# Kernel tuning notes

Measured on AMD Instinct MI355X. Metric: run time of the kernel, lower is better.

## Reference

```python
import jax, jax.numpy as jnp
import numpy as np

K = 1024
D = 64
BETA = 0.25
DECAY = 0.99
EPS = 1e-05


def setup_inputs() -> dict:
    key = jax.random.key(0)
    k1, k2 = jax.random.split(key)
    z = jax.random.normal(k1, (32, D, 64, 64), dtype=jnp.float32)
    # nn.init.uniform_(weight, -1/K, 1/K)
    embedding = jax.random.uniform(k2, (K, D), dtype=jnp.float32, minval=-1.0 / K, maxval=1.0 / K)
    # post-_maybe_init_ema_from_embedding state
    cluster_size = jnp.ones((K,), dtype=jnp.float32)
    embed_avg = embedding.copy()
    return {"z": z, "embedding": embedding, "cluster_size": cluster_size, "embed_avg": embed_avg}


def reference(z, embedding, cluster_size, embed_avg):
    B, C, H, W = z.shape
    z_nhwc = jnp.transpose(z, (0, 2, 3, 1))            # [B,H,W,D]
    flat = z_nhwc.reshape(-1, D)                        # [N,D]

    x2 = jnp.sum(flat * flat, axis=1, keepdims=True)    # [N,1]
    w2 = jnp.sum(embedding * embedding, axis=1)         # [K]
    dist = x2 + w2[None, :] - 2.0 * flat @ embedding.T  # [N,K]
    idx = jnp.argmin(dist, axis=1)                      # [N] int

    z_q = embedding[idx].reshape(z_nhwc.shape)          # gather

    # EMA codebook update (training, update=True)
    counts = jax.ops.segment_sum(jnp.ones_like(idx, dtype=jnp.float32), idx, num_segments=K)
    embed_sum = jax.ops.segment_sum(flat, idx, num_segments=K)  # [K,D]
    new_cluster_size = cluster_size * DECAY + (1.0 - DECAY) * counts
    new_embed_avg = embed_avg * DECAY + (1.0 - DECAY) * embed_sum
    n = jnp.sum(new_cluster_size)
    smoothed = (new_cluster_size + EPS) / (n + K * EPS) * n
    new_embedding = new_embed_avg / smoothed[:, None]

    # commitment loss (z_q detached) + straight-through estimator
    loss = BETA * jnp.mean((z_nhwc - jax.lax.stop_gradient(z_q)) ** 2)
    z_q_ste = z_nhwc + jax.lax.stop_gradient(z_q - z_nhwc)
    z_q_out = jnp.transpose(z_q_ste, (0, 3, 1, 2))      # back to [B,C,H,W]
    return (z_q_out, idx, loss, new_embedding, new_cluster_size, new_embed_avg)
```

## Files before the change

kernel.cpp:

```cpp
#include <hip/hip_runtime.h>
#include <hip/hip_bf16.h>

#define NROWS 131072
#define DDIM  64
#define KCODES 1024
#define HW    4096

#define OFF_ZQ   0ull
#define OFF_IDX  8388608ull
#define OFF_LOSS 8519680ull
#define OFF_EMB  8519681ull
#define OFF_NCS  8585217ull
#define OFF_EAVG 8586241ull

#define SCR_B0    34078724ull
#define SCR_WLO   (SCR_B0 + 131072ull)
#define SCR_W2O   (SCR_B0 + 262144ull)
#define LCAP      20480u

#define FWS_KSCR   16777216ull
#define FWS_ES     16777216ull
#define FWS_CNTF   17039360ull
#define FWS_SX2    17043456ull
#define FWS_SMOOTH 17047552ull
#define FWS_LIST   17301504ull
#define FWS_RMIN   17383424ull
#define FWS_CNTR   17547264ull
#define FWS_TOTAL  17547268ull

#define WSO_KSCR   262144ull
#define WSO_LOSSB  786432ull
#define WSO_SMOOTH 788480ull
#define WSO_CNT    792576ull
#define WSO_ESUM   858112ull

#define GAPTHR 8e-5f

typedef __attribute__((ext_vector_type(8))) short bf16x8;
typedef __attribute__((ext_vector_type(4))) float f32x4;

__device__ __forceinline__ float np_sumsq64(const float* v) {
#pragma clang fp contract(off)
    float r0 = v[0]*v[0], r1 = v[1]*v[1], r2 = v[2]*v[2], r3 = v[3]*v[3];
    float r4 = v[4]*v[4], r5 = v[5]*v[5], r6 = v[6]*v[6], r7 = v[7]*v[7];
    for (int i = 8; i < 64; i += 8) {
        r0 += v[i+0]*v[i+0]; r1 += v[i+1]*v[i+1];
        r2 += v[i+2]*v[i+2]; r3 += v[i+3]*v[i+3];
        r4 += v[i+4]*v[i+4]; r5 += v[i+5]*v[i+5];
        r6 += v[i+6]*v[i+6]; r7 += v[i+7]*v[i+7];
    }
    return ((r0+r1)+(r2+r3))+((r4+r5)+(r6+r7));
}
__device__ __forceinline__ float mul_rn(float a, float b) {
#pragma clang fp contract(off)
    return a * b;
}
__device__ __forceinline__ float add_rn(float a, float b) {
#pragma clang fp contract(off)
    return a + b;
}
__device__ __forceinline__ float sub2_rn(float s, float a) {
#pragma clang fp contract(off)
    return s - 2.0f * a;
}
__device__ __forceinline__ unsigned bf16rne(float v) {
    unsigned b = __float_as_uint(v);
    return (b + 0x7FFFu + ((b >> 16) & 1u)) >> 16;
}
__device__ __forceinline__ float bfu2f(unsigned short u) {
    return __uint_as_float(((unsigned)u) << 16);
}
__device__ __forceinline__ unsigned flipf(float v) {
    unsigned b = __float_as_uint(v);
    return b ^ (0x80000000u | (unsigned)((int)b >> 31));
}
__device__ __forceinline__ float unflip_val(unsigned u) {
    u &= 0xFFFFFC00u;
    unsigned mask = 0x80000000u | (unsigned)((int)(~u) >> 31);
    return __uint_as_float(u ^ mask);
}

__global__ __launch_bounds__(256) void prep_kernel(
        const float* __restrict__ emb, unsigned short* __restrict__ wh,
        unsigned short* __restrict__ wl, float* __restrict__ w2,
        float* __restrict__ embT) {
    __shared__ float tile[64][65];
    const int t = threadIdx.x;
    const int kb = blockIdx.x * 64;
#pragma unroll
    for (int i = 0; i < 16; ++i) {
        const int e = t + i * 256;
        const int kl = e >> 6, d = e & 63;
        const float v = emb[(size_t)(kb + kl) * DDIM + d];
        tile[kl][d] = v;
        const unsigned rh = bf16rne(v);
        const float lv = v - bfu2f((unsigned short)rh);
        wh[(size_t)(kb + kl) * DDIM + d] = (unsigned short)rh;
        wl[(size_t)(kb + kl) * DDIM + d] = (unsigned short)bf16rne(lv);
    }
    __syncthreads();
    if (t < 64) w2[kb + t] = np_sumsq64(&tile[t][0]);
#pragma unroll
    for (int i = 0; i < 16; ++i) {
        const int e = t + i * 256;
        const int d = e >> 6, kl = e & 63;
        embT[(size_t)d * KCODES + kb + kl] = tile[kl][d];
    }
}

#define CBLOAD(S, c)                                                          \
    { const size_t a_ = ((size_t)(((c) * 16 + col) * DDIM + grp * 8));        \
      wh##S##0 = *(const bf16x8*)(wh + a_);                                   \
      wh##S##1 = *(const bf16x8*)(wh + a_ + 32);                              \
      wl##S##0 = *(const bf16x8*)(wl + a_);                                   \
      wl##S##1 = *(const bf16x8*)(wl + a_ + 32); }

#define CBCOMP4(S, c)                                                         \
    { const float4 w2v = *(const float4*)&w2g[(c) * 16 + grp * 4];            \
      const float* w2p = (const float*)&w2v;                                  \
      _Pragma("unroll")                                                       \
      for (int rt = 0; rt < 4; ++rt) {                                        \
        f32x4 aA = {0.f,0.f,0.f,0.f}, aB = {0.f,0.f,0.f,0.f};                 \
        aA = __builtin_amdgcn_mfma_f32_16x16x32_bf16(wh##S##0, fx[rt][0], aA, 0, 0, 0); \
        aA = __builtin_amdgcn_mfma_f32_16x16x32_bf16(wl##S##0, fx[rt][0], aA, 0, 0, 0); \
        aB = __builtin_amdgcn_mfma_f32_16x16x32_bf16(wh##S##1, fx[rt][1], aB, 0, 0, 0); \
        aB = __builtin_amdgcn_mfma_f32_16x16x32_bf16(wl##S##1, fx[rt][1], aB, 0, 0, 0); \
        _Pragma("unroll")                                                     \
        for (int r = 0; r < 4; ++r) {                                         \
          const float val = fmaf(-2.f, aA[r] + aB[r], w2p[r]);                \
          const unsigned u = (flipf(val) & 0xFFFFFC00u) |                     \
                             (unsigned)((c) * 16 + grp * 4 + r);              \
          const unsigned mx = m1[rt] > u ? m1[rt] : u;                        \
          m1[rt] = m1[rt] < u ? m1[rt] : u;                                   \
          m2[rt] = m2[rt] < mx ? m2[rt] : mx;                                 \
        } } }

__global__ __launch_bounds__(512, 4) void score2_kernel(
        const float* __restrict__ z,
        const unsigned short* __restrict__ wh, const unsigned short* __restrict__ wl,
        const float* __restrict__ w2g, float* __restrict__ out,
        unsigned short* __restrict__ xT, unsigned* __restrict__ list,
        unsigned long long* __restrict__ rmin, unsigned* __restrict__ counter) {
    __shared__ __attribute__((aligned(16))) unsigned short sxt[64][512];

    const int tid = threadIdx.x;
    const int lane = tid & 63, wid = tid >> 6;
    const int col = lane & 15, grp = lane >> 4;
    const int nb = blockIdx.x * 512;
    const int b = nb >> 12, hb = (nb >> 6) & 63;

    {
        const int w4 = (tid & 15) * 4, h = (tid >> 4) & 7, dg = tid >> 7;
#pragma unroll
        for (int j = 0; j < 16; ++j) {
            const int d = dg * 16 + j;
            const float4 v = *(const float4*)&z[((size_t)(b * 64 + d)) * HW + (hb + h) * 64 + w4];
            ushort4 u;
            u.x = (unsigned short)bf16rne(v.x);
            u.y = (unsigned short)bf16rne(v.y);
            u.z = (unsigned short)bf16rne(v.z);
            u.w = (unsigned short)bf16rne(v.w);
            *(ushort4*)&sxt[d][h * 64 + w4] = u;
        }
    }
    __syncthreads();

    bf16x8 fx[4][2];
#pragma unroll
    for (int rt = 0; rt < 4; ++rt)
#pragma unroll
        for (int kh = 0; kh < 2; ++kh) {
            const int row = wid * 64 + rt * 16 + col;
            bf16x8 f;
#pragma unroll
            for (int j = 0; j < 8; ++j)
                f[j] = (short)sxt[kh * 32 + grp * 8 + j][row];
            fx[rt][kh] = f;
            *(bf16x8*)&xT[(size_t)(nb + row) * DDIM + kh * 32 + grp * 8] = f;
        }

    unsigned m1[4] = {~0u, ~0u, ~0u, ~0u}, m2[4] = {~0u, ~0u, ~0u, ~0u};
    bf16x8 whA0, whA1, wlA0, wlA1, whB0, whB1, wlB0, wlB1;

    CBLOAD(A, 0)
    for (int c = 0; c < 64; c += 2) {
        CBLOAD(B, c + 1)
        CBCOMP4(A, c)
        if (c + 2 < 64) CBLOAD(A, c + 2)
        CBCOMP4(B, c + 1)
    }

#pragma unroll
    for (int rt = 0; rt < 4; ++rt) {
        for (int off = 16; off <= 32; off <<= 1) {
            const unsigned o1 = (unsigned)__shfl_xor((int)m1[rt], off, 64);
            const unsigned o2 = (unsigned)__shfl_xor((int)m2[rt], off, 64);
            const unsigned mx = m1[rt] > o1 ? m1[rt] : o1;
            m1[rt] = m1[rt] < o1 ? m1[rt] : o1;
            const unsigned t2 = m2[rt] < o2 ? m2[rt] : o2;
            m2[rt] = t2 < mx ? t2 : mx;
        }
    }

    bool flag[4];
    unsigned long long mrt[4];
    unsigned wavecnt = 0;
#pragma unroll
    for (int rt = 0; rt < 4; ++rt) {
        flag[rt] = (grp == 0) &&
                   ((unflip_val(m2[rt]) - unflip_val(m1[rt])) < GAPTHR);
        mrt[rt] = __ballot(flag[rt]);
        wavecnt += (unsigned)__popcll(mrt[rt]);
    }

    if (grp == 0) {
#pragma unroll
        for (int rt = 0; rt < 4; ++rt)
            out[OFF_IDX + (size_t)(nb + wid * 64 + rt * 16 + col)] =
                (float)(m1[rt] & 1023u);
    }

    unsigned base = 0;
    if (lane == 0 && wavecnt) base = atomicAdd(counter, wavecnt);
    base = (unsigned)__shfl((int)base, 0, 64);
    unsigned offrt = 0;
#pragma unroll
    for (int rt = 0; rt < 4; ++rt) {
        if (flag[rt]) {
            const unsigned offin =
                (unsigned)__popcll(mrt[rt] & ((lane == 0) ? 0ull : (~0ull >> (64 - lane))));
            const unsigned slot = base + offrt + offin;
            if (slot < LCAP) {
                list[slot] = (unsigned)(nb + wid * 64 + rt * 16 + col);
                rmin[slot] = ~0ull;
            }
        }
        offrt += (unsigned)__popcll(mrt[rt]);
    }
}

__global__ __launch_bounds__(256, 1) void rescanb_kernel(
        const float* __restrict__ z, const float* __restrict__ emb,
        const float* __restrict__ w2, const unsigned* __restrict__ list,
        const unsigned* __restrict__ counter,
        unsigned long long* __restrict__ rmin) {
    const int lane = threadIdx.x & 63;
    const int wid = __builtin_amdgcn_readfirstlane(threadIdx.x >> 6);
    unsigned cnt = __builtin_amdgcn_readfirstlane(*counter);
    if (cnt > LCAP) cnt = LCAP;
    if (cnt == 0) return;
    const unsigned W = ((cnt + 63) >> 6) * 8;

    for (unsigned w = blockIdx.x * 4 + wid; w < W; w += gridDim.x * 4) {
        const unsigned g = w >> 3, p = w & 7;
        const unsigned slot = g * 64 + lane;
        const bool valid = slot < cnt;
        const unsigned n = list[valid ? slot : 0];
        const unsigned hw = n & 4095u, bb = n >> 12;

        float x[64];
#pragma unroll
        for (int d = 0; d < 64; ++d)
            x[d] = z[(size_t)(bb * 64 + d) * (size_t)HW + hw];

        float r[8];
#pragma unroll
        for (int j = 0; j < 8; ++j) r[j] = mul_rn(x[j], x[j]);
#pragma unroll
        for (int i = 8; i < 64; i += 8)
#pragma unroll
            for (int j = 0; j < 8; ++j)
                r[j] = add_rn(r[j], mul_rn(x[i + j], x[i + j]));
        const float x2 = add_rn(add_rn(add_rn(r[0], r[1]), add_rn(r[2], r[3])),
                                add_rn(add_rn(r[4], r[5]), add_rn(r[6], r[7])));

        unsigned long long best = ~0ull;
        const int k0 = (int)p * 128;
        for (int k = k0; k < k0 + 128; k += 2) {
            const float* wa = emb + (size_t)k * DDIM;
            const float* wb = wa + DDIM;
            float aa = 0.f, ab = 0.f;
#pragma unroll
            for (int d = 0; d < 64; ++d) {
                aa = fmaf(x[d], wa[d], aa);
                ab = fmaf(x[d], wb[d], ab);
            }
            const float da = sub2_rn(add_rn(x2, w2[k]),     aa);
            const float db = sub2_rn(add_rn(x2, w2[k + 1]), ab);
            const unsigned long long ua =
                ((unsigned long long)flipf(da) << 10) | (unsigned long long)k;
            const unsigned long long ub =
                ((unsigned long long)flipf(db) << 10) | (unsigned long long)(k + 1);
            best = best < ua ? best : ua;
            best = best < ub ? best : ub;
        }
        if (valid) atomicMin(&rmin[slot], best);
    }
}

__global__ __launch_bounds__(256) void fix_kernel(
        const unsigned* __restrict__ list, const unsigned long long* __restrict__ rmin,
        const unsigned* __restrict__ counter, float* __restrict__ out) {
    unsigned cnt = *counter;
    if (cnt > LCAP) cnt = LCAP;
    const unsigned t = blockIdx.x * 256 + threadIdx.x;
    if (t < cnt) {
        const unsigned long long u = rmin[t];
        if (u != ~0ull)
            out[OFF_IDX + (size_t)list[t]] = (float)(unsigned)(u & 1023ull);
    }
}

__global__ __launch_bounds__(256) void gather_kernel(
        const float* __restrict__ idxf, const unsigned short* __restrict__ xT,
        float* __restrict__ es, float* __restrict__ cntf, float* __restrict__ sx2a) {
    const int k = blockIdx.x;
    const int lane = threadIdx.x & 63, wid = threadIdx.x >> 6;
    const float fk = (float)k;
    float acc = 0.f, s2 = 0.f;
    unsigned cnt = 0;
    const int wbase = wid * 32768;

    float4 cur = *(const float4*)&idxf[wbase + lane * 4];
    for (int it = 0; it < 128; ++it) {
        float4 nxt;
        if (it + 1 < 128)
            nxt = *(const float4*)&idxf[wbase + (it + 1) * 256 + lane * 4];
        const float* cp = (const float*)&cur;
#pragma unroll
        for (int j = 0; j < 4; ++j) {
            unsigned long long m = __ballot(cp[j] == fk);
            cnt += (unsigned)__popcll(m);
            while (m) {
                const int src = __ffsll(m) - 1;
                m &= m - 1;
                const int n = wbase + it * 256 + src * 4 + j;
                const float xv = bfu2f(xT[(size_t)n * DDIM + lane]);
                acc += xv;
                s2 = fmaf(xv, xv, s2);
            }
        }
        cur = nxt;
    }
#pragma unroll
    for (int off = 32; off > 0; off >>= 1) s2 += __shfl_down(s2, off, 64);
    __shared__ float sacc[4][64];
    __shared__ float ssx2[4];
    __shared__ unsigned scnt[4];
    sacc[wid][lane] = acc;
    if (lane == 0) { ssx2[wid] = s2; scnt[wid] = cnt; }
    __syncthreads();
    if (wid == 0) {
        const float t = sacc[0][lane] + sacc[1][lane] + sacc[2][lane] + sacc[3][lane];
        es[(size_t)k * DDIM + lane] = t;
        if (lane == 0) {
            cntf[k] = (float)(scnt[0] + scnt[1] + scnt[2] + scnt[3]);
            sx2a[k] = ssx2[0] + ssx2[1] + ssx2[2] + ssx2[3];
        }
    }
}

__global__ __launch_bounds__(512, 4) void zq_kernel(
        const float* __restrict__ emb, const float* __restrict__ idxf,
        float* __restrict__ out) {
    __shared__ unsigned k1s[256];
    const int tid = threadIdx.x;
    const int lane = tid & 63, wid = tid >> 6;
    const int nb = blockIdx.x * 256;
    const int b = nb >> 12, hb = (nb >> 6) & 63;
    if (tid < 256) k1s[tid] = (unsigned)idxf[nb + tid];
    __syncthreads();

    const int h = lane >> 4, w4 = (lane & 15) * 4;
    const int row = h * 64 + w4;
    const float* e0 = emb + (size_t)k1s[row + 0] * DDIM;
    const float* e1 = emb + (size_t)k1s[row + 1] * DDIM;
    const float* e2 = emb + (size_t)k1s[row + 2] * DDIM;
    const float* e3 = emb + (size_t)k1s[row + 3] * DDIM;
#pragma unroll
    for (int it = 0; it < 8; ++it) {
        const int d = wid + 8 * it;
        float4 q;
        q.x = e0[d]; q.y = e1[d]; q.z = e2[d]; q.w = e3[d];
        *(float4*)&out[((size_t)(b * 64 + d)) * HW + (hb + h) * 64 + w4] = q;
    }
}

__global__ __launch_bounds__(1024) void fin1_f(
        const float* __restrict__ cs, const float* __restrict__ emb,
        float* __restrict__ out, const float* __restrict__ w2,
        const float* __restrict__ es, const float* __restrict__ cntf,
        const float* __restrict__ sx2a, float* __restrict__ smoothed) {
    const int k = threadIdx.x;
    const float cnt = cntf[k];
    const float w2k = w2[k];
    const float* ek = es + (size_t)k * DDIM;
    const float* wk = emb + (size_t)k * DDIM;
    float dt = 0.f;
#pragma unroll
    for (int d = 0; d < DDIM; ++d) dt = fmaf(ek[d], wk[d], dt);
    const float lp = sx2a[k] - 2.f * dt + cnt * w2k;
    const float ncs = fmaf(0.01f, cnt, 0.99f * cs[k]);

    __shared__ float red[1024];
    red[k] = ncs;
    __syncthreads();
    for (int s = 512; s > 0; s >>= 1) {
        if (k < s) red[k] += red[k + s];
        __syncthreads();
    }
    const float nn = red[0];
    __syncthreads();
    red[k] = lp;
    __syncthreads();
    for (int s = 512; s > 0; s >>= 1) {
        if (k < s) red[k] += red[k + s];
        __syncthreads();
    }
    smoothed[k] = (ncs + 1e-5f) / (nn + 1024.f * 1e-5f) * nn;
    out[OFF_NCS + (size_t)k] = ncs;
    if (k == 0) out[OFF_LOSS] = 0.25f * red[0] / 8388608.f;
}

__global__ __launch_bounds__(256) void fin2_f(
        const float* __restrict__ eavg, float* __restrict__ out,
        const float* __restrict__ es, const float* __restrict__ smoothed) {
    const int e = blockIdx.x * 256 + threadIdx.x;
    const float ea = fmaf(0.01f, es[e], 0.99f * eavg[e]);
    out[OFF_EAVG + (size_t)e] = ea;
    out[OFF_EMB  + (size_t)e] = ea / smoothed[e >> 6];
}


#define CBCOMP(S, c)                                                          \
    { const float4 w2v = *(const float4*)&w2s[(c) * 16 + grp * 4];            \
      const float* w2p = (const float*)&w2v;                                  \
      _Pragma("unroll")                                                       \
      for (int rt = 0; rt < 2; ++rt) {                                        \
        f32x4 aA = {0.f,0.f,0.f,0.f}, aB = {0.f,0.f,0.f,0.f};                 \
        aA = __builtin_amdgcn_mfma_f32_16x16x32_bf16(wh##S##0, fx[rt][0], aA, 0, 0, 0); \
        aA = __builtin_amdgcn_mfma_f32_16x16x32_bf16(wl##S##0, fx[rt][0], aA, 0, 0, 0); \
        aB = __builtin_amdgcn_mfma_f32_16x16x32_bf16(wh##S##1, fx[rt][1], aB, 0, 0, 0); \
        aB = __builtin_amdgcn_mfma_f32_16x16x32_bf16(wl##S##1, fx[rt][1], aB, 0, 0, 0); \
        _Pragma("unroll")                                                     \
        for (int r = 0; r < 4; ++r) {                                         \
          const float val = fmaf(-2.f, aA[r] + aB[r], w2p[r]);                \
          const unsigned u = (flipf(val) & 0xFFFFFC00u) |                     \
                             (unsigned)((c) * 16 + grp * 4 + r);              \
          const unsigned mx = m1[rt] > u ? m1[rt] : u;                        \
          m1[rt] = m1[rt] < u ? m1[rt] : u;                                   \
          m2[rt] = m2[rt] < mx ? m2[rt] : mx;                                 \
        } } }

__global__ __launch_bounds__(512, 4) void score_kernel(
        const float* __restrict__ z,
        const unsigned short* __restrict__ wh, const unsigned short* __restrict__ wl,
        const float* __restrict__ w2, unsigned* __restrict__ kscr) {
    __shared__ __attribute__((aligned(16))) unsigned short sxt[64][260];
    __shared__ float w2s[KCODES];

    const int tid = threadIdx.x;
    const int lane = tid & 63, wid = tid >> 6;
    const int col = lane & 15, grp = lane >> 4;
    const int nb = blockIdx.x * 256;
    const int b = nb >> 12, hb = (nb >> 6) & 63;

    for (int i = tid; i < KCODES; i += 512) w2s[i] = w2[i];
    {
        const int h = lane >> 4, w4 = (lane & 15) * 4;
        const int row = h * 64 + w4;
#pragma unroll
        for (int it = 0; it < 8; ++it) {
            const int d = wid + 8 * it;
            const float4 v = *(const float4*)&z[((size_t)(b * 64 + d)) * HW + (hb + h) * 64 + w4];
            ushort4 u;
            u.x = (unsigned short)bf16rne(v.x);
            u.y = (unsigned short)bf16rne(v.y);
            u.z = (unsigned short)bf16rne(v.z);
            u.w = (unsigned short)bf16rne(v.w);
            *(ushort4*)&sxt[d][row] = u;
        }
    }
    __syncthreads();

    bf16x8 fx[2][2];
#pragma unroll
    for (int rt = 0; rt < 2; ++rt)
#pragma unroll
        for (int kh = 0; kh < 2; ++kh) {
            const int row = wid * 32 + rt * 16 + col;
            bf16x8 f;
#pragma unroll
            for (int j = 0; j < 8; ++j)
                f[j] = (short)sxt[kh * 32 + grp * 8 + j][row];
            fx[rt][kh] = f;
        }

    unsigned m1[2] = {~0u, ~0u}, m2[2] = {~0u, ~0u};
    bf16x8 whA0, whA1, wlA0, wlA1, whB0, whB1, wlB0, wlB1;

    CBLOAD(A, 0)
    for (int c = 0; c < 64; c += 2) {
        CBLOAD(B, c + 1)
        CBCOMP(A, c)
        if (c + 2 < 64) CBLOAD(A, c + 2)
        CBCOMP(B, c + 1)
    }
#pragma unroll
    for (int rt = 0; rt < 2; ++rt) {
        for (int off = 16; off <= 32; off <<= 1) {
            const unsigned o1 = (unsigned)__shfl_xor((int)m1[rt], off, 64);
            const unsigned o2 = (unsigned)__shfl_xor((int)m2[rt], off, 64);
            const unsigned mx = m1[rt] > o1 ? m1[rt] : o1;
            m1[rt] = m1[rt] < o1 ? m1[rt] : o1;
            const unsigned t2 = m2[rt] < o2 ? m2[rt] : o2;
            m2[rt] = t2 < mx ? t2 : mx;
        }
        if (grp == 0) {
            const bool fl = (unflip_val(m2[rt]) - unflip_val(m1[rt])) < GAPTHR;
            kscr[nb + wid * 32 + rt * 16 + col] =
                (m1[rt] & 1023u) | (fl ? 0x80000000u : 0u);
        }
    }
}

__global__ __launch_bounds__(512, 4) void output_kernel(
        const float* __restrict__ z, const float* __restrict__ emb,
        const float* __restrict__ embT, const float* __restrict__ w2,
        float* __restrict__ out, const unsigned* __restrict__ kscr,
        float* __restrict__ esum_p, unsigned* __restrict__ cnt_p,
        float* __restrict__ lossb, int pmask) {
    __shared__ __attribute__((aligned(16))) unsigned short sxt[64][260];
    __shared__ unsigned k1s[256];
    __shared__ float redl[8];

    const int tid = threadIdx.x;
    const int lane = tid & 63, wid = tid >> 6;
    const int nb = blockIdx.x * 256;
    const int b = nb >> 12, hb = (nb >> 6) & 63;

    {
        const int h = lane >> 4, w4 = (lane & 15) * 4;
        const int row = h * 64 + w4;
#pragma unroll
        for (int it = 0; it < 8; ++it) {
            const int d = wid + 8 * it;
            const float4 v = *(const float4*)&z[((size_t)(b * 64 + d)) * HW + (hb + h) * 64 + w4];
            ushort4 u;
            u.x = (unsigned short)bf16rne(v.x);
            u.y = (unsigned short)bf16rne(v.y);
            u.z = (unsigned short)bf16rne(v.z);
            u.w = (unsigned short)bf16rne(v.w);
            *(ushort4*)&sxt[d][row] = u;
        }
    }

    unsigned kf = 0;
    if (lane < 32) kf = kscr[nb + wid * 32 + lane];
    int k1 = (int)(kf & 1023u);
    unsigned long long need = __ballot((lane < 32) && (kf & 0x80000000u));
    while (need) {
        const int src = __ffsll(need) - 1;
        need &= need - 1;
        const int nr = nb + wid * 32 + src;
        const int wq = nr & 63, hq = (nr >> 6) & 63, bq = nr >> 12;
        const float xv = z[(size_t)bq * DDIM * HW + (size_t)lane * HW + hq * 64 + wq];
        const float p = mul_rn(xv, xv);
        float r = 0.f;
        for (int i = 0; i < 8; ++i) {
            const float t = __shfl(p, (i << 3) + (lane & 7), 64);
            r = add_rn(r, t);
        }
        const float s01 = add_rn(r, __shfl_xor(r, 1, 64));
        const float s03 = add_rn(s01, __shfl_xor(s01, 2, 64));
        const float s07 = add_rn(s03, __shfl_xor(s03, 4, 64));
        const float x2s = __shfl(s07, 0, 64);

        float acc[16];
#pragma unroll
        for (int j = 0; j < 16; ++j) acc[j] = 0.f;
        for (int d = 0; d < DDIM; ++d) {
            const float xd = __shfl(xv, d, 64);
            const float* ecol = embT + (size_t)d * KCODES + lane;
#pragma unroll
            for (int j = 0; j < 16; ++j)
                acc[j] = fmaf(ecol[64 * j], xd, acc[j]);
        }
        float bv = 1e30f;
        int bk = KCODES;
#pragma unroll
        for (int j = 0; j < 16; ++j) {
            const int kk = lane + 64 * j;
            const float s  = add_rn(x2s, w2[kk]);
            const float dv = sub2_rn(s, acc[j]);
            if (dv < bv) { bv = dv; bk = kk; }
        }
        for (int off = 32; off > 0; off >>= 1) {
            const float ov = __shfl_xor(bv, off, 64);
            const int   ok = __shfl_xor(bk, off, 64);
            if (ov < bv || (ov == bv && ok < bk)) { bv = ov; bk = ok; }
        }
        if (lane == src) k1 = bk;
    }
    if (lane < 32) k1s[wid * 32 + lane] = (unsigned)k1;
    __syncthreads();

    const int part = blockIdx.x & pmask;
    if (tid < 256) {
        const unsigned myk = k1s[tid];
        out[OFF_IDX + (size_t)(nb + tid)] = (float)myk;
        atomicAdd(&cnt_p[part * KCODES + myk], 1u);
    }

    float ls = 0.f;
    {
        const int h = lane >> 4, w4 = (lane & 15) * 4;
        const int row = h * 64 + w4;
#pragma unroll 2
        for (int it = 0; it < 8; ++it) {
            const int d = wid + 8 * it;
            float4 q;
            float* qp = (float*)&q;
#pragma unroll
            for (int j = 0; j < 4; ++j) {
                const unsigned k = k1s[row + j];
                const float wv = emb[(size_t)k * DDIM + d];
                qp[j] = wv;
                const float diff = bfu2f(sxt[d][row + j]) - wv;
                ls = fmaf(diff, diff, ls);
            }
            *(float4*)&out[((size_t)(b * 64 + d)) * HW + (hb + h) * 64 + w4] = q;
        }
    }
#pragma unroll
    for (int off = 32; off > 0; off >>= 1) ls += __shfl_down(ls, off, 64);
    if (lane == 0) redl[wid] = ls;
    __syncthreads();
    if (tid == 0) {
        float t = 0.f;
#pragma unroll
        for (int i = 0; i < 8; ++i) t += redl[i];
        lossb[blockIdx.x] = t;
    }
    {
        float* ep = esum_p + (size_t)part * 65536;
        for (int r = 0; r < 32; ++r) {
            const int row = wid * 32 + r;
            atomicAdd(&ep[(size_t)k1s[row] * DDIM + lane], bfu2f(sxt[lane][row]));
        }
    }
}

__global__ __launch_bounds__(1024) void finalize1_kernel(
        const float* __restrict__ cs, float* __restrict__ out,
        const unsigned* __restrict__ cnt_p, const float* __restrict__ lossb,
        float* __restrict__ smoothed, int P) {
    const int k = threadIdx.x;
    unsigned c = 0;
    for (int p = 0; p < P; ++p) c += cnt_p[p * KCODES + k];
    const float ncs = fmaf(0.01f, (float)c, 0.99f * cs[k]);

    __shared__ float red[1024];
    red[k] = ncs;
    __syncthreads();
    for (int s = 512; s > 0; s >>= 1) {
        if (k < s) red[k] += red[k + s];
        __syncthreads();
    }
    const float nn = red[0];
    smoothed[k] = (ncs + 1e-5f) / (nn + 1024.f * 1e-5f) * nn;
    out[OFF_NCS + (size_t)k] = ncs;

    __syncthreads();
    red[k] = (k < 512) ? lossb[k] : 0.f;
    __syncthreads();
    for (int s = 512; s > 0; s >>= 1) {
        if (k < s) red[k] += red[k + s];
        __syncthreads();
    }
    if (k == 0) out[OFF_LOSS] = 0.25f * red[0] / 8388608.f;
}

__global__ __launch_bounds__(256) void finalize2_kernel(
        const float* __restrict__ eavg, float* __restrict__ out,
        const float* __restrict__ esum_p, const float* __restrict__ smoothed,
        int P) {
    const int e = blockIdx.x * 256 + threadIdx.x;
    float s = 0.f;
    for (int p = 0; p < P; ++p) s += esum_p[(size_t)p * 65536 + e];
    const float ea = fmaf(0.01f, s, 0.99f * eavg[e]);
    out[OFF_EAVG + (size_t)e] = ea;
    out[OFF_EMB  + (size_t)e] = ea / smoothed[e >> 6];
}


extern "C" void kernel_launch(void* const* d_in, const int* in_sizes, int n_in,
                              void* d_out, int out_size, void* d_ws, size_t ws_size,
                              hipStream_t stream) {
    const float* z    = (const float*)d_in[0];
    const float* emb  = (const float*)d_in[1];
    const float* cs   = (const float*)d_in[2];
    const float* eavg = (const float*)d_in[3];
    float* out = (float*)d_out;

    unsigned short* wh = (unsigned short*)((char*)d_out + SCR_B0);
    unsigned short* wl = (unsigned short*)((char*)d_out + SCR_WLO);
    float*          w2 = (float*)((char*)d_out + SCR_W2O);
    char* ws = (char*)d_ws;

    if (ws_size >= FWS_TOTAL) {
        unsigned short*     xT   = (unsigned short*)ws;
        float*              es   = (float*)(ws + FWS_ES);
        float*              cntf = (float*)(ws + FWS_CNTF);
        float*              sx2a = (float*)(ws + FWS_SX2);
        float*              smoo = (float*)(ws + FWS_SMOOTH);
        unsigned*           list = (unsigned*)(ws + FWS_LIST);
        unsigned long long* rmin = (unsigned long long*)(ws + FWS_RMIN);
        unsigned*           cntr = (unsigned*)(ws + FWS_CNTR);
        float*              embT = (float*)(ws + FWS_KSCR);

        (void)hipMemsetAsync(cntr, 0, 4, stream);
        prep_kernel<<<16, 256, 0, stream>>>(emb, wh, wl, w2, embT);
        score2_kernel<<<NROWS / 512, 512, 0, stream>>>(
            z, wh, wl, w2, out, xT, list, rmin, cntr);
        rescanb_kernel<<<256, 256, 0, stream>>>(z, emb, w2, list, cntr, rmin);
        fix_kernel<<<LCAP / 256, 256, 0, stream>>>(list, rmin, cntr, out);
        zq_kernel<<<NROWS / 256, 512, 0, stream>>>(emb, out + OFF_IDX, out);
        gather_kernel<<<KCODES, 256, 0, stream>>>(out + OFF_IDX, xT, es, cntf, sx2a);
        fin1_f<<<1, 1024, 0, stream>>>(cs, emb, out, w2, es, cntf, sx2a, smoo);
        fin2_f<<<256, 256, 0, stream>>>(eavg, out, es, smoo);
    } else {
        int P = 1;
        for (int p = 16; p >= 1; p >>= 1)
            if (ws_size >= WSO_ESUM + (size_t)p * 262144ull) { P = p; break; }

        float*    embT   = (float*)ws;
        unsigned* kscr   = (unsigned*)(ws + WSO_KSCR);
        float*    lossb  = (float*)(ws + WSO_LOSSB);
        float*    smooth = (float*)(ws + WSO_SMOOTH);
        unsigned* cnt_p  = (unsigned*)(ws + WSO_CNT);
        float*    esum_p = (float*)(ws + WSO_ESUM);

        (void)hipMemsetAsync(ws + WSO_CNT, 0, 65536 + (size_t)P * 262144ull, stream);
        prep_kernel<<<16, 256, 0, stream>>>(emb, wh, wl, w2, embT);
        score_kernel<<<NROWS / 256, 512, 0, stream>>>(z, wh, wl, w2, kscr);
        output_kernel<<<NROWS / 256, 512, 0, stream>>>(
            z, emb, embT, w2, out, kscr, esum_p, cnt_p, lossb, P - 1);
        finalize1_kernel<<<1, 1024, 0, stream>>>(cs, out, cnt_p, lossb, smooth, P);
        finalize2_kernel<<<256, 256, 0, stream>>>(eavg, out, esum_p, smooth, P);
    }
}
```

Baseline: 306.3 us.

## Fuse z_q gather into scoring kernel and patch corrected rows in fix kernel

The separate zq_kernel, which reread the index array and gathered codebook rows into the NCHW output, is removed. The scoring kernel now stages its argmin indices in shared memory and writes z_q directly after a block barrier. The fix kernel now launches one wave per flagged row and rewrites both the index and that row's 64 channels with the rescanned code. This saves a kernel launch and a full pass over the index array, at the cost of a longer scoring kernel, an extra barrier, and z_q values that are written twice for ambiguous rows.

```diff
diff --git a/kernel.cpp b/kernel.cpp
--- a/kernel.cpp
+++ b/kernel.cpp
@@ -136,31 +136,32 @@
         } } }
 
 __global__ __launch_bounds__(512, 4) void score2_kernel(
-        const float* __restrict__ z,
+        const float* __restrict__ z, const float* __restrict__ emb,
         const unsigned short* __restrict__ wh, const unsigned short* __restrict__ wl,
         const float* __restrict__ w2g, float* __restrict__ out,
         unsigned short* __restrict__ xT, unsigned* __restrict__ list,
         unsigned long long* __restrict__ rmin, unsigned* __restrict__ counter) {
     __shared__ __attribute__((aligned(16))) unsigned short sxt[64][512];
+    __shared__ unsigned k1s[512];
 
     const int tid = threadIdx.x;
     const int lane = tid & 63, wid = tid >> 6;
     const int col = lane & 15, grp = lane >> 4;
     const int nb = blockIdx.x * 512;
     const int b = nb >> 12, hb = (nb >> 6) & 63;
+    const int w4 = (tid & 15) * 4, h8 = (tid >> 4) & 7, dg = tid >> 7;
 
     {
-        const int w4 = (tid & 15) * 4, h = (tid >> 4) & 7, dg = tid >> 7;
 #pragma unroll
         for (int j = 0; j < 16; ++j) {
             const int d = dg * 16 + j;
-            const float4 v = *(const float4*)&z[((size_t)(b * 64 + d)) * HW + (hb + h) * 64 + w4];
+            const float4 v = *(const float4*)&z[((size_t)(b * 64 + d)) * HW + (hb + h8) * 64 + w4];
             ushort4 u;
             u.x = (unsigned short)bf16rne(v.x);
             u.y = (unsigned short)bf16rne(v.y);
             u.z = (unsigned short)bf16rne(v.z);
             u.w = (unsigned short)bf16rne(v.w);
-            *(ushort4*)&sxt[d][h * 64 + w4] = u;
+            *(ushort4*)&sxt[d][h8 * 64 + w4] = u;
         }
     }
     __syncthreads();
@@ -215,9 +216,11 @@
 
     if (grp == 0) {
 #pragma unroll
-        for (int rt = 0; rt < 4; ++rt)
-            out[OFF_IDX + (size_t)(nb + wid * 64 + rt * 16 + col)] =
-                (float)(m1[rt] & 1023u);
+        for (int rt = 0; rt < 4; ++rt) {
+            const unsigned k = m1[rt] & 1023u;
+            out[OFF_IDX + (size_t)(nb + wid * 64 + rt * 16 + col)] = (float)k;
+            k1s[wid * 64 + rt * 16 + col] = k;
+        }
     }
 
     unsigned base = 0;
@@ -236,6 +239,22 @@
             }
         }
         offrt += (unsigned)__popcll(mrt[rt]);
+    }
+
+    __syncthreads();
+    {
+        const int r0 = h8 * 64 + w4;
+        const float* e0 = emb + (size_t)k1s[r0 + 0] * DDIM;
+        const float* e1 = emb + (size_t)k1s[r0 + 1] * DDIM;
+        const float* e2 = emb + (size_t)k1s[r0 + 2] * DDIM;
+        const float* e3 = emb + (size_t)k1s[r0 + 3] * DDIM;
+#pragma unroll
+        for (int j = 0; j < 16; ++j) {
+            const int d = dg * 16 + j;
+            float4 q;
+            q.x = e0[d]; q.y = e1[d]; q.z = e2[d]; q.w = e3[d];
+            *(float4*)&out[((size_t)(b * 64 + d)) * HW + (hb + h8) * 64 + w4] = q;
+        }
     }
 }
 
@@ -300,15 +319,20 @@
 
 __global__ __launch_bounds__(256) void fix_kernel(
         const unsigned* __restrict__ list, const unsigned long long* __restrict__ rmin,
-        const unsigned* __restrict__ counter, float* __restrict__ out) {
+        const unsigned* __restrict__ counter, const float* __restrict__ emb,
+        float* __restrict__ out) {
     unsigned cnt = *counter;
     if (cnt > LCAP) cnt = LCAP;
-    const unsigned t = blockIdx.x * 256 + threadIdx.x;
-    if (t < cnt) {
-        const unsigned long long u = rmin[t];
-        if (u != ~0ull)
-            out[OFF_IDX + (size_t)list[t]] = (float)(unsigned)(u & 1023ull);
-    }
+    const int lane = threadIdx.x & 63, ws = threadIdx.x >> 6;
+    const unsigned t = blockIdx.x * 4 + ws;
+    if (t >= cnt) return;
+    const unsigned long long u = rmin[t];
+    if (u == ~0ull) return;
+    const unsigned k = (unsigned)(u & 1023ull);
+    const unsigned n = list[t];
+    if (lane == 0) out[OFF_IDX + (size_t)n] = (float)k;
+    const unsigned hw = n & 4095u, bb = n >> 12;
+    out[((size_t)(bb * 64 + lane)) * HW + hw] = emb[(size_t)k * DDIM + lane];
 }
 
 __global__ __launch_bounds__(256) void gather_kernel(
@@ -357,32 +381,6 @@
             cntf[k] = (float)(scnt[0] + scnt[1] + scnt[2] + scnt[3]);
             sx2a[k] = ssx2[0] + ssx2[1] + ssx2[2] + ssx2[3];
         }
-    }
-}
-
-__global__ __launch_bounds__(512, 4) void zq_kernel(
-        const float* __restrict__ emb, const float* __restrict__ idxf,
-        float* __restrict__ out) {
-    __shared__ unsigned k1s[256];
-    const int tid = threadIdx.x;
-    const int lane = tid & 63, wid = tid >> 6;
-    const int nb = blockIdx.x * 256;
-    const int b = nb >> 12, hb = (nb >> 6) & 63;
-    if (tid < 256) k1s[tid] = (unsigned)idxf[nb + tid];
-    __syncthreads();
-
-    const int h = lane >> 4, w4 = (lane & 15) * 4;
-    const int row = h * 64 + w4;
-    const float* e0 = emb + (size_t)k1s[row + 0] * DDIM;
-    const float* e1 = emb + (size_t)k1s[row + 1] * DDIM;
-    const float* e2 = emb + (size_t)k1s[row + 2] * DDIM;
-    const float* e3 = emb + (size_t)k1s[row + 3] * DDIM;
-#pragma unroll
-    for (int it = 0; it < 8; ++it) {
-        const int d = wid + 8 * it;
-        float4 q;
-        q.x = e0[d]; q.y = e1[d]; q.z = e2[d]; q.w = e3[d];
-        *(float4*)&out[((size_t)(b * 64 + d)) * HW + (hb + h) * 64 + w4] = q;
     }
 }
 
@@ -722,10 +720,9 @@
         (void)hipMemsetAsync(cntr, 0, 4, stream);
         prep_kernel<<<16, 256, 0, stream>>>(emb, wh, wl, w2, embT);
         score2_kernel<<<NROWS / 512, 512, 0, stream>>>(
-            z, wh, wl, w2, out, xT, list, rmin, cntr);
+            z, emb, wh, wl, w2, out, xT, list, rmin, cntr);
         rescanb_kernel<<<256, 256, 0, stream>>>(z, emb, w2, list, cntr, rmin);
-        fix_kernel<<<LCAP / 256, 256, 0, stream>>>(list, rmin, cntr, out);
-        zq_kernel<<<NROWS / 256, 512, 0, stream>>>(emb, out + OFF_IDX, out);
+        fix_kernel<<<LCAP / 4, 256, 0, stream>>>(list, rmin, cntr, emb, out);
         gather_kernel<<<KCODES, 256, 0, stream>>>(out + OFF_IDX, xT, es, cntf, sx2a);
         fin1_f<<<1, 1024, 0, stream>>>(cs, emb, out, w2, es, cntf, sx2a, smoo);
         fin2_f<<<256, 256, 0, stream>>>(eavg, out, es, smoo);
```

New measurement: 302.6 us. Within noise of the previous version (-1.2%).
